# Optimization experiments

Hardware: AMD Instinct MI355X
Metric: run time of the kernel (lower is better)

The kernel has to match this reference:

```python
import jax, jax.numpy as jnp
import numpy as np

IN = 128          # in_channels
STEPS = 3         # processing_steps


def setup_inputs() -> dict:
    key = jax.random.key(0)
    ks = jax.random.split(key, 6)
    N, B = 500000, 1024
    x = jax.random.normal(ks[0], (N, IN), dtype=jnp.float32)
    batch = jnp.sort(jax.random.randint(ks[1], (N,), 0, B)).astype(jnp.int64)
    s = 1.0 / np.sqrt(IN)  # PyTorch LSTM init range
    w_ih = jax.random.uniform(ks[2], (4 * IN, 2 * IN), jnp.float32, -s, s)
    w_hh = jax.random.uniform(ks[3], (4 * IN, IN), jnp.float32, -s, s)
    b_ih = jax.random.uniform(ks[4], (4 * IN,), jnp.float32, -s, s)
    b_hh = jax.random.uniform(ks[5], (4 * IN,), jnp.float32, -s, s)
    return {"x": x, "w_ih": w_ih, "w_hh": w_hh, "b_ih": b_ih, "b_hh": b_hh,
            "batch": batch, "batch_size": B}


def reference(x, w_ih, w_hh, b_ih, b_hh, batch, batch_size):
    h = jnp.zeros((batch_size, IN), x.dtype)
    c = jnp.zeros((batch_size, IN), x.dtype)
    q_star = jnp.zeros((batch_size, 2 * IN), x.dtype)
    for _ in range(STEPS):
        # single-layer LSTM step (PyTorch gate order: i, f, g, o)
        gates = q_star @ w_ih.T + b_ih + h @ w_hh.T + b_hh
        i, f, g, o = jnp.split(gates, 4, axis=-1)
        c = jax.nn.sigmoid(f) * c + jax.nn.sigmoid(i) * jnp.tanh(g)
        h = jax.nn.sigmoid(o) * jnp.tanh(c)
        q = h  # [B, IN]
        # per-graph segment softmax over attention scores
        e = jnp.sum(x * q[batch], axis=-1)                       # [N]
        m = jax.ops.segment_max(e, batch, num_segments=batch_size)
        ex = jnp.exp(e - m[batch])
        denom = jax.ops.segment_sum(ex, batch, num_segments=batch_size)
        a = ex / denom[batch]                                    # [N]
        # weighted segment-sum readout
        r = jax.ops.segment_sum(x * a[:, None], batch, num_segments=batch_size)
        q_star = jnp.concatenate([q, r], axis=-1)                # [B, 2*IN]
    return q_star
```

## Files before the change

kernel.cpp:

```cpp
#include <hip/hip_runtime.h>
#include <math.h>

#define IN_CH 128
#define G4    512
#define K1    256

__device__ __forceinline__ float sigmoidf_(float v){ return 1.f/(1.f + expf(-v)); }

__device__ __forceinline__ float dot4_(float4 a, float4 b){
  return a.x*b.x + a.y*b.y + a.z*b.z + a.w*b.w;
}

__device__ __forceinline__ float reduce16_(float v){
  int t;
  t = __builtin_amdgcn_update_dpp(0, __float_as_int(v), 0xB1, 0xF, 0xF, true);
  v += __int_as_float(t);
  t = __builtin_amdgcn_update_dpp(0, __float_as_int(v), 0x4E, 0xF, 0xF, true);
  v += __int_as_float(t);
  t = __builtin_amdgcn_update_dpp(0, __float_as_int(v), 0x141, 0xF, 0xF, true);
  v += __int_as_float(t);
  t = __builtin_amdgcn_update_dpp(0, __float_as_int(v), 0x140, 0xF, 0xF, true);
  v += __int_as_float(t);
  return v;
}

__device__ __forceinline__ float swz16_(float v){
  return __int_as_float(__builtin_amdgcn_ds_swizzle(__float_as_int(v), 0x401F));
}

__global__ void prologue_kernel(const float* __restrict__ w_ih, const float* __restrict__ w_hh,
                                float* __restrict__ wTih, float* __restrict__ wThh,
                                const int* __restrict__ batch, int N, int B, int* __restrict__ segs,
                                const float* __restrict__ b_ih, const float* __restrict__ b_hh,
                                float* __restrict__ h, float* __restrict__ c, float* __restrict__ qstar){
  int blk = blockIdx.x;
  if (blk < 512){
    int idx = blk*256 + threadIdx.x;
    { int g = idx / K1; int k = idx - g*K1; wTih[k*G4 + g] = w_ih[idx]; }
    if (idx < G4*IN_CH){ int g = idx / IN_CH; int k = idx - g*IN_CH; wThh[k*G4 + g] = w_hh[idx]; }
  } else if (blk < 517){
    int b = (blk - 512)*256 + threadIdx.x;
    if (b > B) return;
    if (b == B){ segs[B] = N; return; }
    int lo = 0, hi = N;
    while (lo < hi){ int mid = (lo + hi) >> 1; if (batch[mid] < b) lo = mid + 1; else hi = mid; }
    segs[b] = lo;
  } else {
    int idx = (blk - 517)*256 + threadIdx.x;
    if (idx >= B*IN_CH) return;
    int b = idx >> 7, ch = idx & 127;
    float iv = sigmoidf_(b_ih[ch]           + b_hh[ch]);
    float gv = tanhf    (b_ih[2*IN_CH + ch] + b_hh[2*IN_CH + ch]);
    float ov = sigmoidf_(b_ih[3*IN_CH + ch] + b_hh[3*IN_CH + ch]);
    float cv = iv*gv;
    float hv = ov*tanhf(cv);
    c[idx] = cv; h[idx] = hv;
    qstar[b*K1 + ch] = hv;
  }
}

__global__ __launch_bounds__(512) void lstm_fused_kernel(
    const float* __restrict__ qstar_in, float* __restrict__ h, float* __restrict__ c,
    const float* __restrict__ wTih, const float* __restrict__ wThh,
    const float* __restrict__ b_ih, const float* __restrict__ b_hh,
    float* __restrict__ qstar_out){
  int g    = threadIdx.x;
  int row0 = blockIdx.x*8;
  __shared__ float qs[8][K1];
  __shared__ float hs[8][IN_CH];
  __shared__ float gs[8][G4];
  for (int t = g; t < 8*K1; t += 512){ int r = t >> 8; int k = t & 255; qs[r][k] = qstar_in[(row0+r)*K1 + k]; }
  for (int t = g; t < 8*IN_CH; t += 512){ int r = t >> 7; int k = t & 127; hs[r][k] = h[(row0+r)*IN_CH + k]; }
  __syncthreads();
  float bias = b_ih[g] + b_hh[g];
  float acc[8];
#pragma unroll
  for (int r = 0; r < 8; ++r) acc[r] = bias;
  for (int k4 = 0; k4 < K1/4; ++k4){
    float w0 = wTih[(4*k4+0)*G4 + g];
    float w1 = wTih[(4*k4+1)*G4 + g];
    float w2 = wTih[(4*k4+2)*G4 + g];
    float w3 = wTih[(4*k4+3)*G4 + g];
#pragma unroll
    for (int r = 0; r < 8; ++r){
      float4 q = *reinterpret_cast<const float4*>(&qs[r][4*k4]);
      acc[r] += q.x*w0 + q.y*w1 + q.z*w2 + q.w*w3;
    }
  }
  for (int k4 = 0; k4 < IN_CH/4; ++k4){
    float w0 = wThh[(4*k4+0)*G4 + g];
    float w1 = wThh[(4*k4+1)*G4 + g];
    float w2 = wThh[(4*k4+2)*G4 + g];
    float w3 = wThh[(4*k4+3)*G4 + g];
#pragma unroll
    for (int r = 0; r < 8; ++r){
      float4 hv = *reinterpret_cast<const float4*>(&hs[r][4*k4]);
      acc[r] += hv.x*w0 + hv.y*w1 + hv.z*w2 + hv.w*w3;
    }
  }
#pragma unroll
  for (int r = 0; r < 8; ++r) gs[r][g] = acc[r];
  __syncthreads();
  for (int t = g; t < 8*IN_CH; t += 512){
    int r = t >> 7, ch = t & 127;
    int idx = (row0+r)*IN_CH + ch;
    float iv = sigmoidf_(gs[r][ch]);
    float fv = sigmoidf_(gs[r][IN_CH + ch]);
    float gv = tanhf(gs[r][2*IN_CH + ch]);
    float ov = sigmoidf_(gs[r][3*IN_CH + ch]);
    float cv = fv*c[idx] + iv*gv;
    float hv = ov*tanhf(cv);
    c[idx] = cv; h[idx] = hv;
    qstar_out[(row0+r)*K1 + ch] = hv;
  }
}

__global__ __launch_bounds__(256) void attn_kernel(const float* __restrict__ x,
    float* __restrict__ qstar, const int* __restrict__ segs){
  int b = blockIdx.x;
  int s = segs[b], ce = segs[b+1];
  int tid = threadIdx.x;
  int wave = tid >> 6, lane = tid & 63;
  int grp = (lane >> 4) & 3, l16 = lane & 15;
  int sid = wave*4 + grp;
  const float4 z4 = make_float4(0.f,0.f,0.f,0.f);
  const float4* x4 = reinterpret_cast<const float4*>(x);
  const float4* q4 = reinterpret_cast<const float4*>(&qstar[(size_t)b*K1]);
  float4 qa = q4[l16], qb = q4[16 + l16];

  float m = -INFINITY, d = 0.f;
  float4 ra = z4, rb = z4;

  int j = s + sid*2;
  float4 a0 = z4, b0 = z4, a1 = z4, b1 = z4;
  if (j < ce){
    const float4* r0 = x4 + (size_t)j*(IN_CH/4);
    a0 = r0[l16]; b0 = r0[16 + l16];
    if (j + 1 < ce){ a1 = r0[32 + l16]; b1 = r0[48 + l16]; }
  }
  while (j < ce){
    int jn = j + 32;
    float4 na0 = z4, nb0 = z4, na1 = z4, nb1 = z4;
    if (jn < ce){
      const float4* rn = x4 + (size_t)jn*(IN_CH/4);
      na0 = rn[l16]; nb0 = rn[16 + l16];
      if (jn + 1 < ce){ na1 = rn[32 + l16]; nb1 = rn[48 + l16]; }
    }
    bool ok1 = (j + 1 < ce);
    float e0 = dot4_(a0, qa) + dot4_(b0, qb);
    float e1 = dot4_(a1, qa) + dot4_(b1, qb);
    e0 = reduce16_(e0);
    e1 = reduce16_(e1);
    e1 = ok1 ? e1 : -INFINITY;
    float em = fmaxf(e0, e1);
    if (em > m){
      float corr = __expf(m - em);
      d *= corr;
      ra.x *= corr; ra.y *= corr; ra.z *= corr; ra.w *= corr;
      rb.x *= corr; rb.y *= corr; rb.z *= corr; rb.w *= corr;
      m = em;
    }
    float p0 = __expf(e0 - m);
    float p1 = __expf(e1 - m);
    d += p0 + p1;
    ra.x += p0*a0.x + p1*a1.x; ra.y += p0*a0.y + p1*a1.y;
    ra.z += p0*a0.z + p1*a1.z; ra.w += p0*a0.w + p1*a1.w;
    rb.x += p0*b0.x + p1*b1.x; rb.y += p0*b0.y + p1*b1.y;
    rb.z += p0*b0.z + p1*b1.z; rb.w += p0*b0.w + p1*b1.w;
    j = jn;
    a0 = na0; b0 = nb0; a1 = na1; b1 = nb1;
  }
  {
    float mo = swz16_(m), dd = swz16_(d);
    float4 rao, rbo;
    rao.x = swz16_(ra.x); rao.y = swz16_(ra.y); rao.z = swz16_(ra.z); rao.w = swz16_(ra.w);
    rbo.x = swz16_(rb.x); rbo.y = swz16_(rb.y); rbo.z = swz16_(rb.z); rbo.w = swz16_(rb.w);
    float mn = fmaxf(m, mo);
    float c1 = (mn == -INFINITY) ? 0.f : __expf(m - mn);
    float c2 = (mn == -INFINITY) ? 0.f : __expf(mo - mn);
    d = d*c1 + dd*c2;
    ra.x = ra.x*c1 + rao.x*c2; ra.y = ra.y*c1 + rao.y*c2;
    ra.z = ra.z*c1 + rao.z*c2; ra.w = ra.w*c1 + rao.w*c2;
    rb.x = rb.x*c1 + rbo.x*c2; rb.y = rb.y*c1 + rbo.y*c2;
    rb.z = rb.z*c1 + rbo.z*c2; rb.w = rb.w*c1 + rbo.w*c2;
    m = mn;
  }
  {
    float mo = __shfl_xor(m, 32), dd = __shfl_xor(d, 32);
    float4 rao, rbo;
    rao.x = __shfl_xor(ra.x, 32); rao.y = __shfl_xor(ra.y, 32);
    rao.z = __shfl_xor(ra.z, 32); rao.w = __shfl_xor(ra.w, 32);
    rbo.x = __shfl_xor(rb.x, 32); rbo.y = __shfl_xor(rb.y, 32);
    rbo.z = __shfl_xor(rb.z, 32); rbo.w = __shfl_xor(rb.w, 32);
    float mn = fmaxf(m, mo);
    float c1 = (mn == -INFINITY) ? 0.f : __expf(m - mn);
    float c2 = (mn == -INFINITY) ? 0.f : __expf(mo - mn);
    d = d*c1 + dd*c2;
    ra.x = ra.x*c1 + rao.x*c2; ra.y = ra.y*c1 + rao.y*c2;
    ra.z = ra.z*c1 + rao.z*c2; ra.w = ra.w*c1 + rao.w*c2;
    rb.x = rb.x*c1 + rbo.x*c2; rb.y = rb.y*c1 + rbo.y*c2;
    rb.z = rb.z*c1 + rbo.z*c2; rb.w = rb.w*c1 + rbo.w*c2;
    m = mn;
  }
  __shared__ float mbuf[4], dbuf[4];
  __shared__ float rbA[4][64], rbB[4][64];
  if (lane < 16){
    *reinterpret_cast<float4*>(&rbA[wave][l16*4]) = ra;
    *reinterpret_cast<float4*>(&rbB[wave][l16*4]) = rb;
    if (l16 == 0){ mbuf[wave] = m; dbuf[wave] = d; }
  }
  __syncthreads();
  if (tid < IN_CH){
    float M = fmaxf(fmaxf(mbuf[0], mbuf[1]), fmaxf(mbuf[2], mbuf[3]));
    float f0 = (M == -INFINITY) ? 0.f : __expf(mbuf[0] - M);
    float f1 = (M == -INFINITY) ? 0.f : __expf(mbuf[1] - M);
    float f2 = (M == -INFINITY) ? 0.f : __expf(mbuf[2] - M);
    float f3 = (M == -INFINITY) ? 0.f : __expf(mbuf[3] - M);
    float v0 = (tid < 64) ? rbA[0][tid] : rbB[0][tid-64];
    float v1 = (tid < 64) ? rbA[1][tid] : rbB[1][tid-64];
    float v2 = (tid < 64) ? rbA[2][tid] : rbB[2][tid-64];
    float v3 = (tid < 64) ? rbA[3][tid] : rbB[3][tid-64];
    float R = v0*f0 + v1*f1 + v2*f2 + v3*f3;
    float D = dbuf[0]*f0 + dbuf[1]*f1 + dbuf[2]*f2 + dbuf[3]*f3;
    qstar[(size_t)b*K1 + IN_CH + tid] = (D > 0.f) ? R/D : 0.f;
  }
}

extern "C" void kernel_launch(void* const* d_in, const int* in_sizes, int n_in,
                              void* d_out, int out_size, void* d_ws, size_t ws_size,
                              hipStream_t stream){
  const float* x     = (const float*)d_in[0];
  const float* w_ih  = (const float*)d_in[1];
  const float* w_hh  = (const float*)d_in[2];
  const float* b_ih  = (const float*)d_in[3];
  const float* b_hh  = (const float*)d_in[4];
  const int*   batch = (const int*)d_in[5];
  int N = in_sizes[0] / IN_CH;
  int B = out_size / K1;
  float* out = (float*)d_out;

  float* ws    = (float*)d_ws;
  float* h     = ws;
  float* c     = h + (size_t)B*IN_CH;
  float* wTih  = c + (size_t)B*IN_CH;
  float* wThh  = wTih + K1*G4;
  int*   segs  = (int*)(wThh + IN_CH*G4);

  prologue_kernel<<<517 + (B*IN_CH + 255)/256, 256, 0, stream>>>(
      w_ih, w_hh, wTih, wThh, batch, N, B, segs, b_ih, b_hh, h, c, out);

  attn_kernel<<<B, 256, 0, stream>>>(x, out, segs);
  for (int step = 1; step < 3; ++step){
    lstm_fused_kernel<<<B/8, 512, 0, stream>>>(out, h, c, wTih, wThh, b_ih, b_hh, out);
    attn_kernel<<<B, 256, 0, stream>>>(x, out, segs);
  }
}
```

Before: 206.6 us.

## Use 8-lane groups per row with two-deep prefetch in attention kernel

The attention kernel now gives each x row to an 8-lane group, each lane holding four float4 chunks, instead of a 16-lane group handling two rows per iteration. Each wave covers eight rows at once and prefetches two iterations ahead, loading clamped indices so no conditional loads are needed. The dot-product reduction drops a DPP step, and the final merge adds an extra swizzle stage. The change is meant to raise memory-level parallelism and remove branchy loads, at the cost of more registers per thread and redundant loads of the clamped last row near segment ends.

```diff
diff --git a/kernel.cpp b/kernel.cpp
--- a/kernel.cpp
+++ b/kernel.cpp
@@ -11,7 +11,7 @@
   return a.x*b.x + a.y*b.y + a.z*b.z + a.w*b.w;
 }
 
-__device__ __forceinline__ float reduce16_(float v){
+__device__ __forceinline__ float reduce8_(float v){
   int t;
   t = __builtin_amdgcn_update_dpp(0, __float_as_int(v), 0xB1, 0xF, 0xF, true);
   v += __int_as_float(t);
@@ -19,11 +19,12 @@
   v += __int_as_float(t);
   t = __builtin_amdgcn_update_dpp(0, __float_as_int(v), 0x141, 0xF, 0xF, true);
   v += __int_as_float(t);
-  t = __builtin_amdgcn_update_dpp(0, __float_as_int(v), 0x140, 0xF, 0xF, true);
-  v += __int_as_float(t);
   return v;
 }
 
+__device__ __forceinline__ float swz8_(float v){
+  return __int_as_float(__builtin_amdgcn_ds_swizzle(__float_as_int(v), 0x201F));
+}
 __device__ __forceinline__ float swz16_(float v){
   return __int_as_float(__builtin_amdgcn_ds_swizzle(__float_as_int(v), 0x401F));
 }
@@ -119,95 +120,93 @@
     float* __restrict__ qstar, const int* __restrict__ segs){
   int b = blockIdx.x;
   int s = segs[b], ce = segs[b+1];
+  int jmax = (ce > 0) ? (ce - 1) : 0;
   int tid = threadIdx.x;
   int wave = tid >> 6, lane = tid & 63;
-  int grp = (lane >> 4) & 3, l16 = lane & 15;
-  int sid = wave*4 + grp;
+  int grp = lane >> 3, l8 = lane & 7;
+  int sid = wave*8 + grp;
   const float4 z4 = make_float4(0.f,0.f,0.f,0.f);
   const float4* x4 = reinterpret_cast<const float4*>(x);
   const float4* q4 = reinterpret_cast<const float4*>(&qstar[(size_t)b*K1]);
-  float4 qa = q4[l16], qb = q4[16 + l16];
+  float4 q0 = q4[l8], q1 = q4[8 + l8], q2 = q4[16 + l8], q3 = q4[24 + l8];
 
   float m = -INFINITY, d = 0.f;
-  float4 ra = z4, rb = z4;
-
-  int j = s + sid*2;
-  float4 a0 = z4, b0 = z4, a1 = z4, b1 = z4;
-  if (j < ce){
-    const float4* r0 = x4 + (size_t)j*(IN_CH/4);
-    a0 = r0[l16]; b0 = r0[16 + l16];
-    if (j + 1 < ce){ a1 = r0[32 + l16]; b1 = r0[48 + l16]; }
-  }
-  while (j < ce){
-    int jn = j + 32;
-    float4 na0 = z4, nb0 = z4, na1 = z4, nb1 = z4;
-    if (jn < ce){
-      const float4* rn = x4 + (size_t)jn*(IN_CH/4);
-      na0 = rn[l16]; nb0 = rn[16 + l16];
-      if (jn + 1 < ce){ na1 = rn[32 + l16]; nb1 = rn[48 + l16]; }
-    }
-    bool ok1 = (j + 1 < ce);
-    float e0 = dot4_(a0, qa) + dot4_(b0, qb);
-    float e1 = dot4_(a1, qa) + dot4_(b1, qb);
-    e0 = reduce16_(e0);
-    e1 = reduce16_(e1);
-    e1 = ok1 ? e1 : -INFINITY;
-    float em = fmaxf(e0, e1);
-    if (em > m){
-      float corr = __expf(m - em);
+  float4 ra = z4, rb = z4, rc = z4, rd = z4;
+
+  int j = s + sid;
+  float4 A0, A1, A2, A3, B0, B1, B2, B3;
+  {
+    int jc0 = (j      < ce) ? j      : jmax;
+    int jc1 = (j + 32 < ce) ? j + 32 : jmax;
+    const float4* r0 = x4 + (size_t)jc0*(IN_CH/4);
+    const float4* r1 = x4 + (size_t)jc1*(IN_CH/4);
+    A0 = r0[l8]; A1 = r0[8 + l8]; A2 = r0[16 + l8]; A3 = r0[24 + l8];
+    B0 = r1[l8]; B1 = r1[8 + l8]; B2 = r1[16 + l8]; B3 = r1[24 + l8];
+  }
+  for (; j < ce; j += 32){
+    int jn = j + 64;
+    int jc = (jn < ce) ? jn : jmax;
+    const float4* rp = x4 + (size_t)jc*(IN_CH/4);
+    float4 C0 = rp[l8], C1 = rp[8 + l8], C2 = rp[16 + l8], C3 = rp[24 + l8];
+
+    float e = dot4_(A0, q0) + dot4_(A1, q1) + dot4_(A2, q2) + dot4_(A3, q3);
+    e = reduce8_(e);
+    if (e > m){
+      float corr = __expf(m - e);
       d *= corr;
       ra.x *= corr; ra.y *= corr; ra.z *= corr; ra.w *= corr;
       rb.x *= corr; rb.y *= corr; rb.z *= corr; rb.w *= corr;
-      m = em;
+      rc.x *= corr; rc.y *= corr; rc.z *= corr; rc.w *= corr;
+      rd.x *= corr; rd.y *= corr; rd.z *= corr; rd.w *= corr;
+      m = e;
     }
-    float p0 = __expf(e0 - m);
-    float p1 = __expf(e1 - m);
-    d += p0 + p1;
-    ra.x += p0*a0.x + p1*a1.x; ra.y += p0*a0.y + p1*a1.y;
-    ra.z += p0*a0.z + p1*a1.z; ra.w += p0*a0.w + p1*a1.w;
-    rb.x += p0*b0.x + p1*b1.x; rb.y += p0*b0.y + p1*b1.y;
-    rb.z += p0*b0.z + p1*b1.z; rb.w += p0*b0.w + p1*b1.w;
-    j = jn;
-    a0 = na0; b0 = nb0; a1 = na1; b1 = nb1;
-  }
-  {
-    float mo = swz16_(m), dd = swz16_(d);
-    float4 rao, rbo;
-    rao.x = swz16_(ra.x); rao.y = swz16_(ra.y); rao.z = swz16_(ra.z); rao.w = swz16_(ra.w);
-    rbo.x = swz16_(rb.x); rbo.y = swz16_(rb.y); rbo.z = swz16_(rb.z); rbo.w = swz16_(rb.w);
-    float mn = fmaxf(m, mo);
-    float c1 = (mn == -INFINITY) ? 0.f : __expf(m - mn);
-    float c2 = (mn == -INFINITY) ? 0.f : __expf(mo - mn);
-    d = d*c1 + dd*c2;
-    ra.x = ra.x*c1 + rao.x*c2; ra.y = ra.y*c1 + rao.y*c2;
-    ra.z = ra.z*c1 + rao.z*c2; ra.w = ra.w*c1 + rao.w*c2;
-    rb.x = rb.x*c1 + rbo.x*c2; rb.y = rb.y*c1 + rbo.y*c2;
-    rb.z = rb.z*c1 + rbo.z*c2; rb.w = rb.w*c1 + rbo.w*c2;
-    m = mn;
-  }
-  {
-    float mo = __shfl_xor(m, 32), dd = __shfl_xor(d, 32);
-    float4 rao, rbo;
-    rao.x = __shfl_xor(ra.x, 32); rao.y = __shfl_xor(ra.y, 32);
-    rao.z = __shfl_xor(ra.z, 32); rao.w = __shfl_xor(ra.w, 32);
-    rbo.x = __shfl_xor(rb.x, 32); rbo.y = __shfl_xor(rb.y, 32);
-    rbo.z = __shfl_xor(rb.z, 32); rbo.w = __shfl_xor(rb.w, 32);
-    float mn = fmaxf(m, mo);
-    float c1 = (mn == -INFINITY) ? 0.f : __expf(m - mn);
-    float c2 = (mn == -INFINITY) ? 0.f : __expf(mo - mn);
-    d = d*c1 + dd*c2;
-    ra.x = ra.x*c1 + rao.x*c2; ra.y = ra.y*c1 + rao.y*c2;
-    ra.z = ra.z*c1 + rao.z*c2; ra.w = ra.w*c1 + rao.w*c2;
-    rb.x = rb.x*c1 + rbo.x*c2; rb.y = rb.y*c1 + rbo.y*c2;
-    rb.z = rb.z*c1 + rbo.z*c2; rb.w = rb.w*c1 + rbo.w*c2;
-    m = mn;
-  }
+    float p = __expf(e - m);
+    d += p;
+    ra.x += p*A0.x; ra.y += p*A0.y; ra.z += p*A0.z; ra.w += p*A0.w;
+    rb.x += p*A1.x; rb.y += p*A1.y; rb.z += p*A1.z; rb.w += p*A1.w;
+    rc.x += p*A2.x; rc.y += p*A2.y; rc.z += p*A2.z; rc.w += p*A2.w;
+    rd.x += p*A3.x; rd.y += p*A3.y; rd.z += p*A3.z; rd.w += p*A3.w;
+    A0 = B0; A1 = B1; A2 = B2; A3 = B3;
+    B0 = C0; B1 = C1; B2 = C2; B3 = C3;
+  }
+
+#define MERGE_STAGE(GET)                                                        \
+  {                                                                             \
+    float mo = GET(m), dd = GET(d);                                             \
+    float4 sa, sb, sc, sd;                                                      \
+    sa.x = GET(ra.x); sa.y = GET(ra.y); sa.z = GET(ra.z); sa.w = GET(ra.w);     \
+    sb.x = GET(rb.x); sb.y = GET(rb.y); sb.z = GET(rb.z); sb.w = GET(rb.w);     \
+    sc.x = GET(rc.x); sc.y = GET(rc.y); sc.z = GET(rc.z); sc.w = GET(rc.w);     \
+    sd.x = GET(rd.x); sd.y = GET(rd.y); sd.z = GET(rd.z); sd.w = GET(rd.w);     \
+    float mn = fmaxf(m, mo);                                                    \
+    float c1 = (mn == -INFINITY) ? 0.f : __expf(m - mn);                        \
+    float c2 = (mn == -INFINITY) ? 0.f : __expf(mo - mn);                       \
+    d = d*c1 + dd*c2;                                                           \
+    ra.x = ra.x*c1 + sa.x*c2; ra.y = ra.y*c1 + sa.y*c2;                         \
+    ra.z = ra.z*c1 + sa.z*c2; ra.w = ra.w*c1 + sa.w*c2;                         \
+    rb.x = rb.x*c1 + sb.x*c2; rb.y = rb.y*c1 + sb.y*c2;                         \
+    rb.z = rb.z*c1 + sb.z*c2; rb.w = rb.w*c1 + sb.w*c2;                         \
+    rc.x = rc.x*c1 + sc.x*c2; rc.y = rc.y*c1 + sc.y*c2;                         \
+    rc.z = rc.z*c1 + sc.z*c2; rc.w = rc.w*c1 + sc.w*c2;                         \
+    rd.x = rd.x*c1 + sd.x*c2; rd.y = rd.y*c1 + sd.y*c2;                         \
+    rd.z = rd.z*c1 + sd.z*c2; rd.w = rd.w*c1 + sd.w*c2;                         \
+    m = mn;                                                                     \
+  }
+#define SHFL32(v) __shfl_xor((v), 32)
+  MERGE_STAGE(swz8_)
+  MERGE_STAGE(swz16_)
+  MERGE_STAGE(SHFL32)
+#undef MERGE_STAGE
+#undef SHFL32
+
   __shared__ float mbuf[4], dbuf[4];
-  __shared__ float rbA[4][64], rbB[4][64];
-  if (lane < 16){
-    *reinterpret_cast<float4*>(&rbA[wave][l16*4]) = ra;
-    *reinterpret_cast<float4*>(&rbB[wave][l16*4]) = rb;
-    if (l16 == 0){ mbuf[wave] = m; dbuf[wave] = d; }
+  __shared__ float rbuf[4][IN_CH];
+  if (lane < 8){
+    *reinterpret_cast<float4*>(&rbuf[wave][ 0 + lane*4]) = ra;
+    *reinterpret_cast<float4*>(&rbuf[wave][32 + lane*4]) = rb;
+    *reinterpret_cast<float4*>(&rbuf[wave][64 + lane*4]) = rc;
+    *reinterpret_cast<float4*>(&rbuf[wave][96 + lane*4]) = rd;
+    if (lane == 0){ mbuf[wave] = m; dbuf[wave] = d; }
   }
   __syncthreads();
   if (tid < IN_CH){
@@ -216,11 +215,7 @@
     float f1 = (M == -INFINITY) ? 0.f : __expf(mbuf[1] - M);
     float f2 = (M == -INFINITY) ? 0.f : __expf(mbuf[2] - M);
     float f3 = (M == -INFINITY) ? 0.f : __expf(mbuf[3] - M);
-    float v0 = (tid < 64) ? rbA[0][tid] : rbB[0][tid-64];
-    float v1 = (tid < 64) ? rbA[1][tid] : rbB[1][tid-64];
-    float v2 = (tid < 64) ? rbA[2][tid] : rbB[2][tid-64];
-    float v3 = (tid < 64) ? rbA[3][tid] : rbB[3][tid-64];
-    float R = v0*f0 + v1*f1 + v2*f2 + v3*f3;
+    float R = rbuf[0][tid]*f0 + rbuf[1][tid]*f1 + rbuf[2][tid]*f2 + rbuf[3][tid]*f3;
     float D = dbuf[0]*f0 + dbuf[1]*f1 + dbuf[2]*f2 + dbuf[3]*f3;
     qstar[(size_t)b*K1 + IN_CH + tid] = (D > 0.f) ? R/D : 0.f;
   }
```

Result: faster. 199.5 us (median of 2 runs) (-3.4%).

## Restructure attention loop to 32-lane rows with triple-buffered 4-row loads

Applied to the files above, without the earlier changes.

The attention kernel now assigns one row to each half-wave (32 lanes, one float4 per lane), where before each 16-lane group covered two half-rows. Each wave processes 8 rows per stage across three rotating register buffers, so more independent loads are in flight and global memory latency is better hidden. Out-of-range rows are handled by clamping the load index to the last valid row and masking the scores to -inf, which removes divergent load branches. The cost is more registers per lane and an extra swizzle step in the per-row reduction, though the cross-group merge step shrinks.

```diff
diff --git a/kernel.cpp b/kernel.cpp
--- a/kernel.cpp
+++ b/kernel.cpp
@@ -11,7 +11,7 @@
   return a.x*b.x + a.y*b.y + a.z*b.z + a.w*b.w;
 }
 
-__device__ __forceinline__ float reduce16_(float v){
+__device__ __forceinline__ float reduce32_(float v){
   int t;
   t = __builtin_amdgcn_update_dpp(0, __float_as_int(v), 0xB1, 0xF, 0xF, true);
   v += __int_as_float(t);
@@ -21,11 +21,8 @@
   v += __int_as_float(t);
   t = __builtin_amdgcn_update_dpp(0, __float_as_int(v), 0x140, 0xF, 0xF, true);
   v += __int_as_float(t);
-  return v;
-}
-
-__device__ __forceinline__ float swz16_(float v){
-  return __int_as_float(__builtin_amdgcn_ds_swizzle(__float_as_int(v), 0x401F));
+  t = __builtin_amdgcn_ds_swizzle(__float_as_int(v), 0x401F);
+  return v + __int_as_float(t);
 }
 
 __global__ void prologue_kernel(const float* __restrict__ w_ih, const float* __restrict__ w_hh,
@@ -119,95 +116,100 @@
     float* __restrict__ qstar, const int* __restrict__ segs){
   int b = blockIdx.x;
   int s = segs[b], ce = segs[b+1];
+  int jmax = (ce > 0) ? (ce - 1) : 0;
   int tid = threadIdx.x;
   int wave = tid >> 6, lane = tid & 63;
-  int grp = (lane >> 4) & 3, l16 = lane & 15;
-  int sid = wave*4 + grp;
-  const float4 z4 = make_float4(0.f,0.f,0.f,0.f);
+  int hh = lane >> 5, l32 = lane & 31;
   const float4* x4 = reinterpret_cast<const float4*>(x);
   const float4* q4 = reinterpret_cast<const float4*>(&qstar[(size_t)b*K1]);
-  float4 qa = q4[l16], qb = q4[16 + l16];
+  float4 qv = q4[l32];
 
   float m = -INFINITY, d = 0.f;
-  float4 ra = z4, rb = z4;
-
-  int j = s + sid*2;
-  float4 a0 = z4, b0 = z4, a1 = z4, b1 = z4;
-  if (j < ce){
-    const float4* r0 = x4 + (size_t)j*(IN_CH/4);
-    a0 = r0[l16]; b0 = r0[16 + l16];
-    if (j + 1 < ce){ a1 = r0[32 + l16]; b1 = r0[48 + l16]; }
-  }
-  while (j < ce){
-    int jn = j + 32;
-    float4 na0 = z4, nb0 = z4, na1 = z4, nb1 = z4;
-    if (jn < ce){
-      const float4* rn = x4 + (size_t)jn*(IN_CH/4);
-      na0 = rn[l16]; nb0 = rn[16 + l16];
-      if (jn + 1 < ce){ na1 = rn[32 + l16]; nb1 = rn[48 + l16]; }
-    }
-    bool ok1 = (j + 1 < ce);
-    float e0 = dot4_(a0, qa) + dot4_(b0, qb);
-    float e1 = dot4_(a1, qa) + dot4_(b1, qb);
-    e0 = reduce16_(e0);
-    e1 = reduce16_(e1);
-    e1 = ok1 ? e1 : -INFINITY;
-    float em = fmaxf(e0, e1);
-    if (em > m){
-      float corr = __expf(m - em);
-      d *= corr;
-      ra.x *= corr; ra.y *= corr; ra.z *= corr; ra.w *= corr;
-      rb.x *= corr; rb.y *= corr; rb.z *= corr; rb.w *= corr;
-      m = em;
-    }
-    float p0 = __expf(e0 - m);
-    float p1 = __expf(e1 - m);
-    d += p0 + p1;
-    ra.x += p0*a0.x + p1*a1.x; ra.y += p0*a0.y + p1*a1.y;
-    ra.z += p0*a0.z + p1*a1.z; ra.w += p0*a0.w + p1*a1.w;
-    rb.x += p0*b0.x + p1*b1.x; rb.y += p0*b0.y + p1*b1.y;
-    rb.z += p0*b0.z + p1*b1.z; rb.w += p0*b0.w + p1*b1.w;
-    j = jn;
-    a0 = na0; b0 = nb0; a1 = na1; b1 = nb1;
-  }
+  float4 acc = make_float4(0.f,0.f,0.f,0.f);
+
+  const int WSTR = 32;
+  int jw = s + wave*8;
+
+  float4 A0,A1,A2,A3, B0,B1,B2,B3, C0,C1,C2,C3;
+
+#define LOADW(R0,R1,R2,R3,WB_)                                   \
+  {                                                              \
+    int r0 = min((WB_) + 0 + hh, jmax);                          \
+    int r1 = min((WB_) + 2 + hh, jmax);                          \
+    int r2 = min((WB_) + 4 + hh, jmax);                          \
+    int r3 = min((WB_) + 6 + hh, jmax);                          \
+    R0 = x4[(size_t)r0*(IN_CH/4) + l32];                         \
+    R1 = x4[(size_t)r1*(IN_CH/4) + l32];                         \
+    R2 = x4[(size_t)r2*(IN_CH/4) + l32];                         \
+    R3 = x4[(size_t)r3*(IN_CH/4) + l32];                         \
+  }
+
+#define COMP(R0,R1,R2,R3,WB_)                                    \
+  {                                                              \
+    float e0 = dot4_(R0, qv);                                    \
+    float e1 = dot4_(R1, qv);                                    \
+    float e2 = dot4_(R2, qv);                                    \
+    float e3 = dot4_(R3, qv);                                    \
+    e0 = reduce32_(e0); e1 = reduce32_(e1);                      \
+    e2 = reduce32_(e2); e3 = reduce32_(e3);                      \
+    e0 = ((WB_) + 0 + hh < ce) ? e0 : -INFINITY;                 \
+    e1 = ((WB_) + 2 + hh < ce) ? e1 : -INFINITY;                 \
+    e2 = ((WB_) + 4 + hh < ce) ? e2 : -INFINITY;                 \
+    e3 = ((WB_) + 6 + hh < ce) ? e3 : -INFINITY;                 \
+    float em = fmaxf(fmaxf(e0,e1), fmaxf(e2,e3));                \
+    if (em > m){                                                 \
+      float corr = __expf(m - em);                               \
+      d *= corr;                                                 \
+      acc.x *= corr; acc.y *= corr; acc.z *= corr; acc.w *= corr;\
+      m = em;                                                    \
+    }                                                            \
+    float p0 = (e0 == -INFINITY) ? 0.f : __expf(e0 - m);         \
+    float p1 = (e1 == -INFINITY) ? 0.f : __expf(e1 - m);         \
+    float p2 = (e2 == -INFINITY) ? 0.f : __expf(e2 - m);         \
+    float p3 = (e3 == -INFINITY) ? 0.f : __expf(e3 - m);         \
+    d += (p0 + p1) + (p2 + p3);                                  \
+    acc.x += p0*R0.x + p1*R1.x + p2*R2.x + p3*R3.x;              \
+    acc.y += p0*R0.y + p1*R1.y + p2*R2.y + p3*R3.y;              \
+    acc.z += p0*R0.z + p1*R1.z + p2*R2.z + p3*R3.z;              \
+    acc.w += p0*R0.w + p1*R1.w + p2*R2.w + p3*R3.w;              \
+  }
+
+  LOADW(A0,A1,A2,A3, jw)
+  LOADW(B0,B1,B2,B3, jw + WSTR)
+  for (;;){
+    if (jw >= ce) break;
+    LOADW(C0,C1,C2,C3, jw + 2*WSTR)
+    COMP (A0,A1,A2,A3, jw)
+    jw += WSTR;
+    if (jw >= ce) break;
+    LOADW(A0,A1,A2,A3, jw + 2*WSTR)
+    COMP (B0,B1,B2,B3, jw)
+    jw += WSTR;
+    if (jw >= ce) break;
+    LOADW(B0,B1,B2,B3, jw + 2*WSTR)
+    COMP (C0,C1,C2,C3, jw)
+    jw += WSTR;
+  }
+#undef LOADW
+#undef COMP
+
   {
-    float mo = swz16_(m), dd = swz16_(d);
-    float4 rao, rbo;
-    rao.x = swz16_(ra.x); rao.y = swz16_(ra.y); rao.z = swz16_(ra.z); rao.w = swz16_(ra.w);
-    rbo.x = swz16_(rb.x); rbo.y = swz16_(rb.y); rbo.z = swz16_(rb.z); rbo.w = swz16_(rb.w);
+    float mo = __shfl_xor(m, 32), dd = __shfl_xor(d, 32);
+    float ox = __shfl_xor(acc.x, 32), oy = __shfl_xor(acc.y, 32);
+    float oz = __shfl_xor(acc.z, 32), ow = __shfl_xor(acc.w, 32);
     float mn = fmaxf(m, mo);
     float c1 = (mn == -INFINITY) ? 0.f : __expf(m - mn);
     float c2 = (mn == -INFINITY) ? 0.f : __expf(mo - mn);
     d = d*c1 + dd*c2;
-    ra.x = ra.x*c1 + rao.x*c2; ra.y = ra.y*c1 + rao.y*c2;
-    ra.z = ra.z*c1 + rao.z*c2; ra.w = ra.w*c1 + rao.w*c2;
-    rb.x = rb.x*c1 + rbo.x*c2; rb.y = rb.y*c1 + rbo.y*c2;
-    rb.z = rb.z*c1 + rbo.z*c2; rb.w = rb.w*c1 + rbo.w*c2;
+    acc.x = acc.x*c1 + ox*c2; acc.y = acc.y*c1 + oy*c2;
+    acc.z = acc.z*c1 + oz*c2; acc.w = acc.w*c1 + ow*c2;
     m = mn;
   }
-  {
-    float mo = __shfl_xor(m, 32), dd = __shfl_xor(d, 32);
-    float4 rao, rbo;
-    rao.x = __shfl_xor(ra.x, 32); rao.y = __shfl_xor(ra.y, 32);
-    rao.z = __shfl_xor(ra.z, 32); rao.w = __shfl_xor(ra.w, 32);
-    rbo.x = __shfl_xor(rb.x, 32); rbo.y = __shfl_xor(rb.y, 32);
-    rbo.z = __shfl_xor(rb.z, 32); rbo.w = __shfl_xor(rb.w, 32);
-    float mn = fmaxf(m, mo);
-    float c1 = (mn == -INFINITY) ? 0.f : __expf(m - mn);
-    float c2 = (mn == -INFINITY) ? 0.f : __expf(mo - mn);
-    d = d*c1 + dd*c2;
-    ra.x = ra.x*c1 + rao.x*c2; ra.y = ra.y*c1 + rao.y*c2;
-    ra.z = ra.z*c1 + rao.z*c2; ra.w = ra.w*c1 + rao.w*c2;
-    rb.x = rb.x*c1 + rbo.x*c2; rb.y = rb.y*c1 + rbo.y*c2;
-    rb.z = rb.z*c1 + rbo.z*c2; rb.w = rb.w*c1 + rbo.w*c2;
-    m = mn;
-  }
   __shared__ float mbuf[4], dbuf[4];
-  __shared__ float rbA[4][64], rbB[4][64];
-  if (lane < 16){
-    *reinterpret_cast<float4*>(&rbA[wave][l16*4]) = ra;
-    *reinterpret_cast<float4*>(&rbB[wave][l16*4]) = rb;
-    if (l16 == 0){ mbuf[wave] = m; dbuf[wave] = d; }
+  __shared__ float rbuf[4][IN_CH];
+  if (lane < 32){
+    *reinterpret_cast<float4*>(&rbuf[wave][l32*4]) = acc;
+    if (l32 == 0){ mbuf[wave] = m; dbuf[wave] = d; }
   }
   __syncthreads();
   if (tid < IN_CH){
@@ -216,11 +218,7 @@
     float f1 = (M == -INFINITY) ? 0.f : __expf(mbuf[1] - M);
     float f2 = (M == -INFINITY) ? 0.f : __expf(mbuf[2] - M);
     float f3 = (M == -INFINITY) ? 0.f : __expf(mbuf[3] - M);
-    float v0 = (tid < 64) ? rbA[0][tid] : rbB[0][tid-64];
-    float v1 = (tid < 64) ? rbA[1][tid] : rbB[1][tid-64];
-    float v2 = (tid < 64) ? rbA[2][tid] : rbB[2][tid-64];
-    float v3 = (tid < 64) ? rbA[3][tid] : rbB[3][tid-64];
-    float R = v0*f0 + v1*f1 + v2*f2 + v3*f3;
+    float R = rbuf[0][tid]*f0 + rbuf[1][tid]*f1 + rbuf[2][tid]*f2 + rbuf[3][tid]*f3;
     float D = dbuf[0]*f0 + dbuf[1]*f1 + dbuf[2]*f2 + dbuf[3]*f3;
     qstar[(size_t)b*K1 + IN_CH + tid] = (D > 0.f) ? R/D : 0.f;
   }
```

Result: faster. 200.1 us (-3.1%).
